# Optimization experiments

Measured on AMD Instinct MI355X. Metric: run time of the kernel, lower is better.

## Reference

```python
import jax, jax.numpy as jnp
import numpy as np

N, M, K = 131072, 32, 16
EPS64 = 2.220446049250313e-16  # np.finfo(np.float64).eps, as in the original


def setup_inputs() -> dict:
    key = jax.random.key(0)
    k1, k2, k3, k4, k5 = jax.random.split(key, 5)
    X = jax.random.normal(k1, (N, M), dtype=jnp.float32)
    Wk0 = jax.random.normal(k2, (K,), dtype=jnp.float32)
    W = jax.random.normal(k3, (M, K, K), dtype=jnp.float32)
    mu = jax.random.uniform(k4, (K, K), minval=-4.0, maxval=4.0, dtype=jnp.float32)
    sigma = 0.5 + 0.5 * jax.random.uniform(k5, (K, K), dtype=jnp.float32)
    return {"X": X, "Wk0": Wk0, "W": W, "mu": mu, "sigma": sigma}


def reference(X, Wk0, W, mu, sigma):
    # Softmax-normalized TT weights (original: softmax(Wk0), softmax(W, axis=1))
    z = jax.nn.softmax(Wk0)          # (K,)
    Wn = jax.nn.softmax(W, axis=1)   # (M, K, K)
    inv_norm = 1.0 / (sigma * jnp.sqrt(2.0 * jnp.pi))  # (K, K) Gaussian normalizer

    def step(v, inp):
        # v: (N, K) running left-product z @ resT_0 @ ... @ resT_{i-1}
        x_i, w_i = inp               # x_i: (N,), w_i: (K, K)
        d = (x_i[:, None, None] - mu) / sigma          # (N, K, K)
        B = jnp.exp(-0.5 * d * d) * inv_norm           # Normal(mu, sigma).prob(x)
        res = w_i[None, :, :] * B                      # res[n,a,b] == original res[a,b,n]
        # original: products = products @ res.T, so v_new[n,b] = sum_a v[n,a] * res[n,b,a]
        v_new = jnp.einsum('na,nba->nb', v, res)
        return v_new, None

    v0 = jnp.broadcast_to(z, (X.shape[0], z.shape[0]))   # z @ identity start
    v_final, _ = jax.lax.scan(step, v0, (X.T, Wn))       # scan over M steps
    likelihoods = jnp.sum(v_final, axis=1)               # sum(z @ products, axis=1)
    return jnp.log(likelihoods + EPS64)
```

## Files before the change

kernel.cpp:

```cpp
#include <hip/hip_runtime.h>
#include <cmath>


#define TT_N 131072
#define TT_M 32

typedef float v2f __attribute__((ext_vector_type(2)));
typedef float v4f __attribute__((ext_vector_type(4)));

#define WS_Z 0
#define WS_P 16
#define WS_Q (16 + 256)
#define WS_R (16 + 512)
#define TBL_FLOATS (512 + 8192)

__global__ __launch_bounds__(512) void tt_prep(const float* __restrict__ Wk0,
                                               const float* __restrict__ W,
                                               const float* __restrict__ mu,
                                               const float* __restrict__ sigma,
                                               float* __restrict__ ws) {
    const int t = threadIdx.x;
    const float LOG2E = 1.4426950408889634f;
    const float SCALE = 8388608.0f;
    const float BIAS  = 126.94242f;
    float* z  = ws + WS_Z;
    float* PP = ws + WS_P;
    float* QQ = ws + WS_Q;
    float* RT = ws + WS_R;

    if (t < 16) {
        float mx = -1e30f;
        for (int i = 0; i < 16; ++i) mx = fmaxf(mx, Wk0[i]);
        float se = 0.f;
        for (int i = 0; i < 16; ++i) se += __expf(Wk0[i] - mx);
        z[t] = __expf(Wk0[t] - mx) / se;
    }

    if (t < 256) {
        const int a = t >> 4, b = t & 15;
        float s  = sigma[b * 16 + a];
        float mm = mu[b * 16 + a];
        float c2 = 0.72134752044448f / (s * s);
        PP[a * 16 + b] = -c2 * SCALE;
        QQ[a * 16 + b] = 2.0f * c2 * mm * SCALE;
    }

    const int m = t >> 4;
    const int a = t & 15;
    const float* Wc = W + m * 256 + a;
    float mx = -1e30f;
    #pragma unroll
    for (int b = 0; b < 16; ++b) mx = fmaxf(mx, Wc[b * 16]);
    float se = 0.f;
    #pragma unroll
    for (int b = 0; b < 16; ++b) se += __expf(Wc[b * 16] - mx);
    float lse = __log2f(se);
    #pragma unroll
    for (int b = 0; b < 16; ++b) {
        float s     = sigma[b * 16 + a];
        float mm    = mu[b * 16 + a];
        float inv_s = 1.0f / s;
        float c2    = 0.72134752044448f / (s * s);
        float lw    = (Wc[b * 16] - mx) * LOG2E - lse;
        float R = lw + __log2f(inv_s * 0.3989422804014327f) - c2 * mm * mm;
        RT[m * 256 + a * 16 + b] = (R + BIAS) * SCALE;
    }
}

template <int CTRL>
static __device__ __forceinline__ v2f dpp_v2f(v2f x) {
    v2f r;
    r.x = __int_as_float(
        __builtin_amdgcn_mov_dpp(__float_as_int(x.x), CTRL, 0xF, 0xF, 1));
    r.y = __int_as_float(
        __builtin_amdgcn_mov_dpp(__float_as_int(x.y), CTRL, 0xF, 0xF, 1));
    return r;
}

static __device__ __forceinline__ v2f pk_fma_c0(v2f a, v2f b, v2f c) {
    v2f d;
    asm("v_pk_fma_f32 %0, %1, %2, %3 op_sel:[0,0,0] op_sel_hi:[0,1,0]"
        : "=v"(d) : "v"(a), "v"(b), "v"(c));
    return d;
}
static __device__ __forceinline__ v2f pk_fma_c1(v2f a, v2f b, v2f c) {
    v2f d;
    asm("v_pk_fma_f32 %0, %1, %2, %3 op_sel:[1,0,1] op_sel_hi:[1,1,1]"
        : "=v"(d) : "v"(a), "v"(b), "v"(c));
    return d;
}
static __device__ __forceinline__ v2f pk_fma_a0(v2f a, v2f b, v2f c) {
    v2f d;
    asm("v_pk_fma_f32 %0, %1, %2, %3 op_sel:[0,0,0] op_sel_hi:[0,1,1]"
        : "=v"(d) : "v"(a), "v"(b), "v"(c));
    return d;
}
static __device__ __forceinline__ v2f pk_fma_a1(v2f a, v2f b, v2f c) {
    v2f d;
    asm("v_pk_fma_f32 %0, %1, %2, %3 op_sel:[1,0,0] op_sel_hi:[1,1,1]"
        : "=v"(d) : "v"(a), "v"(b), "v"(c));
    return d;
}

static __device__ __forceinline__ float cvt_exp(float s) {
    unsigned u;
    asm("v_cvt_u32_f32 %0, %1" : "=v"(u) : "v"(s));
    return __uint_as_float(u);
}

__global__ __launch_bounds__(512) void tt_main(const float* __restrict__ X,
                                               const float* __restrict__ ws,
                                               float* __restrict__ out) {
    __shared__ float lds[TBL_FLOATS];
    {
        const v4f* src = (const v4f*)(ws + WS_P);
        v4f* dst = (v4f*)lds;
        for (int i = threadIdx.x; i < TBL_FLOATS / 4; i += 512) dst[i] = src[i];
    }
    __syncthreads();

    const int tid  = blockIdx.x * 512 + threadIdx.x;
    const int pr   = tid >> 2;
    const int n0   = pr * 2;
    const int g    = tid & 3;
    const int boff = g << 2;
    const bool hi1 = (g & 1) != 0;
    const bool hi2 = (g & 2) != 0;

    const float* zp = ws + WS_Z;
    v2f v[16];
    #pragma unroll
    for (int a = 0; a < 16; ++a) v[a] = (v2f){zp[a], zp[a]};

    const float* xp0 = X + (size_t)n0 * TT_M;
    const float* xp1 = xp0 + TT_M;
    v2f S = (v2f){1.f, 1.f};
    v2f xn = (v2f){xp0[0], xp1[0]};

    #pragma unroll 1
    for (int m = 0; m < TT_M; ++m) {
        const v2f xx = xn;
        const int mn = (m + 1 < TT_M) ? m + 1 : m;
        xn = (v2f){xp0[mn], xp1[mn]};
        const v2f xx2 = xx * xx;

        int lo = 0;
        asm volatile("" : "+v"(lo));
        const float* Pm = lds + lo;
        const float* Qm = lds + 256 + lo;
        const float* Rm = lds + 512 + m * 256 + boff + lo;

        v2f acc0 = {0.f, 0.f}, acc1 = {0.f, 0.f};
        v2f acc2 = {0.f, 0.f}, acc3 = {0.f, 0.f};

        #pragma unroll
        for (int a = 0; a < 16; ++a) {
            const v2f va2 = v[a];
            v4f P4 = *(const v4f*)(Pm + a * 16 + boff);
            v4f Q4 = *(const v4f*)(Qm + a * 16 + boff);
            v4f R4 = *(const v4f*)(Rm + a * 16);
            v2f s0 = pk_fma_a0(P4.xy, xx2, pk_fma_c0(Q4.xy, xx, R4.xy));
            v2f s1 = pk_fma_a1(P4.xy, xx2, pk_fma_c1(Q4.xy, xx, R4.xy));
            v2f s2 = pk_fma_a0(P4.zw, xx2, pk_fma_c0(Q4.zw, xx, R4.zw));
            v2f s3 = pk_fma_a1(P4.zw, xx2, pk_fma_c1(Q4.zw, xx, R4.zw));
            acc0.x = __fmaf_rn(va2.x, cvt_exp(s0.x), acc0.x);
            acc0.y = __fmaf_rn(va2.y, cvt_exp(s0.y), acc0.y);
            acc1.x = __fmaf_rn(va2.x, cvt_exp(s1.x), acc1.x);
            acc1.y = __fmaf_rn(va2.y, cvt_exp(s1.y), acc1.y);
            acc2.x = __fmaf_rn(va2.x, cvt_exp(s2.x), acc2.x);
            acc2.y = __fmaf_rn(va2.y, cvt_exp(s2.y), acc2.y);
            acc3.x = __fmaf_rn(va2.x, cvt_exp(s3.x), acc3.x);
            acc3.y = __fmaf_rn(va2.y, cvt_exp(s3.y), acc3.y);
        }

        v2f r0 = dpp_v2f<0xB1>(acc0), r1 = dpp_v2f<0xB1>(acc1);
        v2f r2 = dpp_v2f<0xB1>(acc2), r3 = dpp_v2f<0xB1>(acc3);
        v2f u0 = hi1 ? r0 : acc0;  v2f u1 = hi1 ? r1 : acc1;
        v2f u2 = hi1 ? r2 : acc2;  v2f u3 = hi1 ? r3 : acc3;
        v2f u4 = hi1 ? acc0 : r0;  v2f u5 = hi1 ? acc1 : r1;
        v2f u6 = hi1 ? acc2 : r2;  v2f u7 = hi1 ? acc3 : r3;
        v2f w0 = dpp_v2f<0x4E>(u0), w1 = dpp_v2f<0x4E>(u1);
        v2f w2 = dpp_v2f<0x4E>(u2), w3 = dpp_v2f<0x4E>(u3);
        v2f w4 = dpp_v2f<0x4E>(u4), w5 = dpp_v2f<0x4E>(u5);
        v2f w6 = dpp_v2f<0x4E>(u6), w7 = dpp_v2f<0x4E>(u7);
        v[0]  = hi2 ? w0 : u0;  v[1]  = hi2 ? w1 : u1;
        v[2]  = hi2 ? w2 : u2;  v[3]  = hi2 ? w3 : u3;
        v[4]  = hi2 ? w4 : u4;  v[5]  = hi2 ? w5 : u5;
        v[6]  = hi2 ? w6 : u6;  v[7]  = hi2 ? w7 : u7;
        v[8]  = hi2 ? u0 : w0;  v[9]  = hi2 ? u1 : w1;
        v[10] = hi2 ? u2 : w2;  v[11] = hi2 ? u3 : w3;
        v[12] = hi2 ? u4 : w4;  v[13] = hi2 ? u5 : w5;
        v[14] = hi2 ? u6 : w6;  v[15] = hi2 ? u7 : w7;

        v2f q0 = (v[0] + v[1]) + (v[2] + v[3]);
        v2f q1 = (v[4] + v[5]) + (v[6] + v[7]);
        v2f q2 = (v[8] + v[9]) + (v[10] + v[11]);
        v2f q3 = (v[12] + v[13]) + (v[14] + v[15]);
        S = (q0 + q1) + (q2 + q3);
        if (__all(fmaxf(S.x, S.y) < 5e-17f)) break;
    }

    const float eps = 2.2204460492503131e-16f;
    if (g == 0) {
        out[n0]     = logf(S.x + eps);
        out[n0 + 1] = logf(S.y + eps);
    }
}

extern "C" void kernel_launch(void* const* d_in, const int* in_sizes, int n_in,
                              void* d_out, int out_size, void* d_ws, size_t ws_size,
                              hipStream_t stream) {
    const float* X     = (const float*)d_in[0];
    const float* Wk0   = (const float*)d_in[1];
    const float* W     = (const float*)d_in[2];
    const float* mu    = (const float*)d_in[3];
    const float* sigma = (const float*)d_in[4];
    float* out = (float*)d_out;
    float* ws  = (float*)d_ws;

    tt_prep<<<1, 512, 0, stream>>>(Wk0, W, mu, sigma, ws);
    tt_main<<<(TT_N / 2 * 4) / 512, 512, 0, stream>>>(X, ws, out);
}
```

Baseline: 83.01 us.

## Keep distributed state per lane and broadcast via DPP, unroll steps by two

Each lane now holds only its own four b-components of the running vector instead of all sixteen. The other lanes' values are fetched with a quad_perm DPP broadcast inside the a-loop, which replaces the post-step transpose made of selects and DPP moves. Two M steps are unrolled per iteration with A/B ping-pong buffers, X is loaded as float2 pairs, and the early-exit sum is reduced across lanes with DPP adds every two steps. This cuts register pressure and shuffle overhead, but the early-exit check now runs less often.

```diff
diff --git a/kernel.cpp b/kernel.cpp
--- a/kernel.cpp
+++ b/kernel.cpp
@@ -68,12 +68,15 @@
 }
 
 template <int CTRL>
+static __device__ __forceinline__ float dpp_f(float x) {
+    return __int_as_float(
+        __builtin_amdgcn_mov_dpp(__float_as_int(x), CTRL, 0xF, 0xF, 1));
+}
+template <int CTRL>
 static __device__ __forceinline__ v2f dpp_v2f(v2f x) {
     v2f r;
-    r.x = __int_as_float(
-        __builtin_amdgcn_mov_dpp(__float_as_int(x.x), CTRL, 0xF, 0xF, 1));
-    r.y = __int_as_float(
-        __builtin_amdgcn_mov_dpp(__float_as_int(x.y), CTRL, 0xF, 0xF, 1));
+    r.x = dpp_f<CTRL>(x.x);
+    r.y = dpp_f<CTRL>(x.y);
     return r;
 }
 
@@ -106,6 +109,56 @@
     unsigned u;
     asm("v_cvt_u32_f32 %0, %1" : "=v"(u) : "v"(s));
     return __uint_as_float(u);
+}
+
+template <int H>
+static __device__ __forceinline__ void a_group(const v2f* __restrict__ prev,
+                                               v2f& n0, v2f& n1, v2f& n2, v2f& n3,
+                                               v2f xx, v2f xx2,
+                                               const float* __restrict__ Pm,
+                                               const float* __restrict__ Qm,
+                                               const float* __restrict__ Rm,
+                                               int boff) {
+    #pragma unroll
+    for (int j = 0; j < 4; ++j) {
+        const int a = H * 4 + j;
+        const v2f va2 = dpp_v2f<H * 0x55>(prev[j]);
+        v4f P4 = *(const v4f*)(Pm + a * 16 + boff);
+        v4f Q4 = *(const v4f*)(Qm + a * 16 + boff);
+        v4f R4 = *(const v4f*)(Rm + a * 16);
+        v2f s0 = pk_fma_a0(P4.xy, xx2, pk_fma_c0(Q4.xy, xx, R4.xy));
+        v2f s1 = pk_fma_a1(P4.xy, xx2, pk_fma_c1(Q4.xy, xx, R4.xy));
+        v2f s2 = pk_fma_a0(P4.zw, xx2, pk_fma_c0(Q4.zw, xx, R4.zw));
+        v2f s3 = pk_fma_a1(P4.zw, xx2, pk_fma_c1(Q4.zw, xx, R4.zw));
+        n0.x = __fmaf_rn(va2.x, cvt_exp(s0.x), n0.x);
+        n0.y = __fmaf_rn(va2.y, cvt_exp(s0.y), n0.y);
+        n1.x = __fmaf_rn(va2.x, cvt_exp(s1.x), n1.x);
+        n1.y = __fmaf_rn(va2.y, cvt_exp(s1.y), n1.y);
+        n2.x = __fmaf_rn(va2.x, cvt_exp(s2.x), n2.x);
+        n2.y = __fmaf_rn(va2.y, cvt_exp(s2.y), n2.y);
+        n3.x = __fmaf_rn(va2.x, cvt_exp(s3.x), n3.x);
+        n3.y = __fmaf_rn(va2.y, cvt_exp(s3.y), n3.y);
+    }
+}
+
+static __device__ __forceinline__ void tt_step(const v2f* __restrict__ prev,
+                                               v2f* __restrict__ next,
+                                               v2f xx,
+                                               const float* __restrict__ lds,
+                                               int m, int boff) {
+    const v2f xx2 = xx * xx;
+    int lo = 0;
+    asm volatile("" : "+v"(lo));
+    const float* Pm = lds + lo;
+    const float* Qm = lds + 256 + lo;
+    const float* Rm = lds + 512 + m * 256 + boff + lo;
+
+    v2f n0 = {0.f, 0.f}, n1 = {0.f, 0.f}, n2 = {0.f, 0.f}, n3 = {0.f, 0.f};
+    a_group<0>(prev, n0, n1, n2, n3, xx, xx2, Pm, Qm, Rm, boff);
+    a_group<1>(prev, n0, n1, n2, n3, xx, xx2, Pm, Qm, Rm, boff);
+    a_group<2>(prev, n0, n1, n2, n3, xx, xx2, Pm, Qm, Rm, boff);
+    a_group<3>(prev, n0, n1, n2, n3, xx, xx2, Pm, Qm, Rm, boff);
+    next[0] = n0; next[1] = n1; next[2] = n2; next[3] = n3;
 }
 
 __global__ __launch_bounds__(512) void tt_main(const float* __restrict__ X,
@@ -121,89 +174,48 @@
 
     const int tid  = blockIdx.x * 512 + threadIdx.x;
     const int pr   = tid >> 2;
-    const int n0   = pr * 2;
+    const int n0s  = pr * 2;
     const int g    = tid & 3;
     const int boff = g << 2;
-    const bool hi1 = (g & 1) != 0;
-    const bool hi2 = (g & 2) != 0;
 
     const float* zp = ws + WS_Z;
-    v2f v[16];
-    #pragma unroll
-    for (int a = 0; a < 16; ++a) v[a] = (v2f){zp[a], zp[a]};
-
-    const float* xp0 = X + (size_t)n0 * TT_M;
+    v2f A[4], B[4];
+    #pragma unroll
+    for (int j = 0; j < 4; ++j) A[j] = (v2f){zp[boff + j], zp[boff + j]};
+
+    const float* xp0 = X + (size_t)n0s * TT_M;
     const float* xp1 = xp0 + TT_M;
     v2f S = (v2f){1.f, 1.f};
-    v2f xn = (v2f){xp0[0], xp1[0]};
+    v2f c0 = *(const v2f*)xp0;
+    v2f c1 = *(const v2f*)xp1;
 
     #pragma unroll 1
-    for (int m = 0; m < TT_M; ++m) {
-        const v2f xx = xn;
-        const int mn = (m + 1 < TT_M) ? m + 1 : m;
-        xn = (v2f){xp0[mn], xp1[mn]};
-        const v2f xx2 = xx * xx;
-
-        int lo = 0;
-        asm volatile("" : "+v"(lo));
-        const float* Pm = lds + lo;
-        const float* Qm = lds + 256 + lo;
-        const float* Rm = lds + 512 + m * 256 + boff + lo;
-
-        v2f acc0 = {0.f, 0.f}, acc1 = {0.f, 0.f};
-        v2f acc2 = {0.f, 0.f}, acc3 = {0.f, 0.f};
-
-        #pragma unroll
-        for (int a = 0; a < 16; ++a) {
-            const v2f va2 = v[a];
-            v4f P4 = *(const v4f*)(Pm + a * 16 + boff);
-            v4f Q4 = *(const v4f*)(Qm + a * 16 + boff);
-            v4f R4 = *(const v4f*)(Rm + a * 16);
-            v2f s0 = pk_fma_a0(P4.xy, xx2, pk_fma_c0(Q4.xy, xx, R4.xy));
-            v2f s1 = pk_fma_a1(P4.xy, xx2, pk_fma_c1(Q4.xy, xx, R4.xy));
-            v2f s2 = pk_fma_a0(P4.zw, xx2, pk_fma_c0(Q4.zw, xx, R4.zw));
-            v2f s3 = pk_fma_a1(P4.zw, xx2, pk_fma_c1(Q4.zw, xx, R4.zw));
-            acc0.x = __fmaf_rn(va2.x, cvt_exp(s0.x), acc0.x);
-            acc0.y = __fmaf_rn(va2.y, cvt_exp(s0.y), acc0.y);
-            acc1.x = __fmaf_rn(va2.x, cvt_exp(s1.x), acc1.x);
-            acc1.y = __fmaf_rn(va2.y, cvt_exp(s1.y), acc1.y);
-            acc2.x = __fmaf_rn(va2.x, cvt_exp(s2.x), acc2.x);
-            acc2.y = __fmaf_rn(va2.y, cvt_exp(s2.y), acc2.y);
-            acc3.x = __fmaf_rn(va2.x, cvt_exp(s3.x), acc3.x);
-            acc3.y = __fmaf_rn(va2.y, cvt_exp(s3.y), acc3.y);
-        }
-
-        v2f r0 = dpp_v2f<0xB1>(acc0), r1 = dpp_v2f<0xB1>(acc1);
-        v2f r2 = dpp_v2f<0xB1>(acc2), r3 = dpp_v2f<0xB1>(acc3);
-        v2f u0 = hi1 ? r0 : acc0;  v2f u1 = hi1 ? r1 : acc1;
-        v2f u2 = hi1 ? r2 : acc2;  v2f u3 = hi1 ? r3 : acc3;
-        v2f u4 = hi1 ? acc0 : r0;  v2f u5 = hi1 ? acc1 : r1;
-        v2f u6 = hi1 ? acc2 : r2;  v2f u7 = hi1 ? acc3 : r3;
-        v2f w0 = dpp_v2f<0x4E>(u0), w1 = dpp_v2f<0x4E>(u1);
-        v2f w2 = dpp_v2f<0x4E>(u2), w3 = dpp_v2f<0x4E>(u3);
-        v2f w4 = dpp_v2f<0x4E>(u4), w5 = dpp_v2f<0x4E>(u5);
-        v2f w6 = dpp_v2f<0x4E>(u6), w7 = dpp_v2f<0x4E>(u7);
-        v[0]  = hi2 ? w0 : u0;  v[1]  = hi2 ? w1 : u1;
-        v[2]  = hi2 ? w2 : u2;  v[3]  = hi2 ? w3 : u3;
-        v[4]  = hi2 ? w4 : u4;  v[5]  = hi2 ? w5 : u5;
-        v[6]  = hi2 ? w6 : u6;  v[7]  = hi2 ? w7 : u7;
-        v[8]  = hi2 ? u0 : w0;  v[9]  = hi2 ? u1 : w1;
-        v[10] = hi2 ? u2 : w2;  v[11] = hi2 ? u3 : w3;
-        v[12] = hi2 ? u4 : w4;  v[13] = hi2 ? u5 : w5;
-        v[14] = hi2 ? u6 : w6;  v[15] = hi2 ? u7 : w7;
-
-        v2f q0 = (v[0] + v[1]) + (v[2] + v[3]);
-        v2f q1 = (v[4] + v[5]) + (v[6] + v[7]);
-        v2f q2 = (v[8] + v[9]) + (v[10] + v[11]);
-        v2f q3 = (v[12] + v[13]) + (v[14] + v[15]);
-        S = (q0 + q1) + (q2 + q3);
+    for (int mo = 0; mo < 16; ++mo) {
+        const int nx = (2 * mo + 2 < TT_M) ? 2 * mo + 2 : TT_M - 2;
+        v2f c0n = *(const v2f*)(xp0 + nx);
+        v2f c1n = *(const v2f*)(xp1 + nx);
+
+        const v2f xE = (v2f){c0.x, c1.x};
+        const v2f xO = (v2f){c0.y, c1.y};
+
+        tt_step(A, B, xE, lds, 2 * mo, boff);
+        tt_step(B, A, xO, lds, 2 * mo + 1, boff);
+
+        v2f part = (A[0] + A[1]) + (A[2] + A[3]);
+        part.x += dpp_f<0xB1>(part.x);
+        part.y += dpp_f<0xB1>(part.y);
+        part.x += dpp_f<0x4E>(part.x);
+        part.y += dpp_f<0x4E>(part.y);
+        S = part;
         if (__all(fmaxf(S.x, S.y) < 5e-17f)) break;
+
+        c0 = c0n; c1 = c1n;
     }
 
     const float eps = 2.2204460492503131e-16f;
     if (g == 0) {
-        out[n0]     = logf(S.x + eps);
-        out[n0 + 1] = logf(S.y + eps);
+        out[n0s]     = logf(S.x + eps);
+        out[n0s + 1] = logf(S.y + eps);
     }
 }
 
```

Result: no change. 81.78 us (-1.5%).
